# Kernel optimization log

Hardware: AMD Instinct MI355X
Metric: run time of the kernel (lower is better)

The kernel has to match this reference:

```python
import jax, jax.numpy as jnp
import numpy as np

ALG = 8  # octonion algebra dimension
_TRIPLES = [(1,2,3),(1,4,5),(1,7,6),(2,4,6),(2,5,7),(3,4,7),(3,6,5)]

def _oct_table():
    # Cayley multiplication table: e_i * e_j = S[i,j] * e_{K[i,j]}
    K = np.zeros((8,8), np.int64); S = np.zeros((8,8), np.int64)
    K[0,:] = np.arange(8); S[0,:] = 1
    K[:,0] = np.arange(8); S[:,0] = 1
    for i in range(1,8):
        K[i,i] = 0; S[i,i] = -1
    for (a,b,c) in _TRIPLES:
        for x,y,z in ((a,b,c),(b,c,a),(c,a,b)):
            K[x,y] = z; S[x,y] = 1
            K[y,x] = z; S[y,x] = -1
    return K, S

_K, _S = _oct_table()

def _ternary(w):
    # BitNet-style absmean ternary quantization (STE is irrelevant for fwd)
    scale = jnp.mean(jnp.abs(w)) + 1e-8
    wq = jnp.clip(jnp.round(w / scale), -1.0, 1.0) * scale
    return w + jax.lax.stop_gradient(wq - w)

def _oct_big(w):
    # w: [8, din8, dout8] -> structured dense [8*din8, 8*dout8]
    # out_k = sum_{i,j: e_i e_j = s e_k} s * x_i @ W_j  (64 static blocks)
    din8, dout8 = w.shape[1], w.shape[2]
    big = jnp.zeros((8, din8, 8, dout8), w.dtype)
    for i in range(8):
        for j in range(8):
            big = big.at[i, :, int(_K[i, j]), :].set(float(_S[i, j]) * w[j])
    return big.reshape(8 * din8, 8 * dout8)

def _oct_linear(x, w):
    return x @ _oct_big(_ternary(w))

def setup_inputs() -> dict:
    key = jax.random.key(0)
    k1, k2, k3, k4 = jax.random.split(key, 4)
    B, T, D = 8, 4096, 768
    H = 2048  # int(2*4*768/3) rounded up to multiple of 8
    d8, h8 = D // ALG, H // ALG
    x = jax.random.normal(k1, (B, T, D), dtype=jnp.float32)
    w_gate = 0.02 * jax.random.normal(k2, (ALG, d8, h8), dtype=jnp.float32)
    w_up   = 0.02 * jax.random.normal(k3, (ALG, d8, h8), dtype=jnp.float32)
    w_down = 0.02 * jax.random.normal(k4, (ALG, h8, d8), dtype=jnp.float32)
    return {"x": x, "w_gate": w_gate, "w_up": w_up, "w_down": w_down}

def reference(x, w_gate, w_up, w_down):
    gate = _oct_linear(x, w_gate)          # [B,T,H]
    up   = _oct_linear(x, w_up)            # [B,T,H]
    h    = jax.nn.silu(gate) * up          # SwiGLU gate
    return _oct_linear(h, w_down)          # [B,T,D]
```

## Files before the change

kernel.cpp:

```cpp
#include <hip/hip_runtime.h>
#include <hip/hip_bf16.h>

typedef unsigned short u16;
typedef unsigned int u32;
typedef float f32x4 __attribute__((ext_vector_type(4)));
typedef __bf16 bf16x8 __attribute__((ext_vector_type(8)));

#define AS1 __attribute__((address_space(1)))
#define AS3 __attribute__((address_space(3)))

#define MTOT 32768
#define DK   768
#define HN   2048

__constant__ signed char J_TAB[64] = {
  0,1,2,3,4,5,6,7,
  1,0,3,2,5,4,7,6,
  2,3,0,1,6,7,4,5,
  3,2,1,0,7,6,5,4,
  4,5,6,7,0,1,2,3,
  5,4,7,6,1,0,3,2,
  6,7,4,5,2,3,0,1,
  7,6,5,4,3,2,1,0};
__constant__ signed char S_TAB[64] = {
   1, 1, 1, 1, 1, 1, 1, 1,
  -1, 1,-1, 1,-1, 1, 1,-1,
  -1, 1, 1,-1,-1,-1, 1, 1,
  -1,-1, 1, 1,-1, 1,-1, 1,
  -1, 1, 1, 1, 1,-1,-1,-1,
  -1,-1, 1,-1, 1, 1, 1,-1,
  -1,-1,-1, 1, 1,-1, 1, 1,
  -1, 1,-1,-1, 1, 1,-1, 1};

__device__ __forceinline__ u16 f2bf(float f) {
  u32 x = __float_as_uint(f);
  x += 0x7fffu + ((x >> 16) & 1u);
  return (u16)(x >> 16);
}

__device__ __forceinline__ void gload_lds16(const void* g, void* l) {
  __builtin_amdgcn_global_load_lds((AS1 void*)(g), (AS3 void*)(l), 16, 0, 0);
}

#define PVMW(N) do { __builtin_amdgcn_sched_barrier(0); \
  asm volatile("s_waitcnt vmcnt(" #N ")" ::: "memory"); \
  __builtin_amdgcn_sched_barrier(0); } while (0)
#define PBAR() do { __builtin_amdgcn_sched_barrier(0); \
  __builtin_amdgcn_s_barrier(); \
  __builtin_amdgcn_sched_barrier(0); } while (0)
#define VMW(N) asm volatile("s_waitcnt vmcnt(" #N ")" ::: "memory")
#define BAR() __builtin_amdgcn_s_barrier()

template <int LDK>
__device__ __forceinline__ void stage_half(const u16* __restrict__ src,
                                           u16* lds, int tid) {
#pragma unroll
  for (int f0 = 0; f0 < 1024; f0 += 512) {
    int flat = f0 + tid;
    int row = flat >> 3;
    int c = (flat & 7) ^ (row & 7);
    gload_lds16(src + row * LDK + c * 8, lds + (f0 + (tid & ~63)) * 8);
  }
}

template <int LDK, bool SA, bool SB, int VM>
__device__ __forceinline__ void ktile4(
    const u16* lAp, const u16* lBp, u16* lAn, u16* lBn,
    const u16* __restrict__ aStage, const u16* __restrict__ bStage,
    int tid, int arow, int brow, int c0, int c1, f32x4 (&acc)[8][4]) {
  bf16x8 a0[4], a1[4], a2[4], a3[4], b0[4], b1[4];
#pragma unroll
  for (int mi = 0; mi < 4; ++mi)
    a0[mi] = *(const bf16x8*)(lAp + (arow + mi * 16) * 64 + c0);
#pragma unroll
  for (int ni = 0; ni < 4; ++ni)
    b0[ni] = *(const bf16x8*)(lBp + (brow + ni * 16) * 64 + c0);
#pragma unroll
  for (int mi = 0; mi < 4; ++mi)
    a1[mi] = *(const bf16x8*)(lAp + (arow + mi * 16) * 64 + c1);
#pragma unroll
  for (int ni = 0; ni < 4; ++ni)
    b1[ni] = *(const bf16x8*)(lBp + (brow + ni * 16) * 64 + c1);
  if constexpr (SA) stage_half<LDK>(aStage, lAn, tid);
  PBAR();
  __builtin_amdgcn_s_setprio(1);
#pragma unroll
  for (int mi = 0; mi < 4; ++mi)
#pragma unroll
    for (int ni = 0; ni < 4; ++ni)
      acc[mi][ni] = __builtin_amdgcn_mfma_f32_16x16x32_bf16(
          a0[mi], b0[ni], acc[mi][ni], 0, 0, 0);
  __builtin_amdgcn_s_setprio(0);
  PBAR();
#pragma unroll
  for (int mi = 0; mi < 4; ++mi)
    a2[mi] = *(const bf16x8*)(lAp + (arow + 64 + mi * 16) * 64 + c0);
  if constexpr (SA) stage_half<LDK>(aStage + 128 * LDK, lAn + 128 * 64, tid);
  PBAR();
  __builtin_amdgcn_s_setprio(1);
#pragma unroll
  for (int mi = 0; mi < 4; ++mi)
#pragma unroll
    for (int ni = 0; ni < 4; ++ni)
      acc[mi][ni] = __builtin_amdgcn_mfma_f32_16x16x32_bf16(
          a1[mi], b1[ni], acc[mi][ni], 0, 0, 0);
  __builtin_amdgcn_s_setprio(0);
  PBAR();
#pragma unroll
  for (int mi = 0; mi < 4; ++mi)
    a3[mi] = *(const bf16x8*)(lAp + (arow + 64 + mi * 16) * 64 + c1);
  if constexpr (SB) stage_half<LDK>(bStage, lBn, tid);
  PBAR();
  __builtin_amdgcn_s_setprio(1);
#pragma unroll
  for (int mi = 0; mi < 4; ++mi)
#pragma unroll
    for (int ni = 0; ni < 4; ++ni)
      acc[4 + mi][ni] = __builtin_amdgcn_mfma_f32_16x16x32_bf16(
          a2[mi], b0[ni], acc[4 + mi][ni], 0, 0, 0);
  __builtin_amdgcn_s_setprio(0);
  PBAR();
  if constexpr (SB) stage_half<LDK>(bStage + 128 * LDK, lBn + 128 * 64, tid);
  if constexpr (VM == 4) PVMW(4);
  else if constexpr (VM == 0) PVMW(0);
  PBAR();
  __builtin_amdgcn_s_setprio(1);
#pragma unroll
  for (int mi = 0; mi < 4; ++mi)
#pragma unroll
    for (int ni = 0; ni < 4; ++ni)
      acc[4 + mi][ni] = __builtin_amdgcn_mfma_f32_16x16x32_bf16(
          a3[mi], b1[ni], acc[4 + mi][ni], 0, 0, 0);
  __builtin_amdgcn_s_setprio(0);
  PBAR();
}

template <int NK, int LDK>
__device__ __forceinline__ void gemm_core(const u16* __restrict__ aSrc,
                                          const u16* __restrict__ bSrc, int tid,
                                          u16* lA0, u16* lA1, u16* lB0, u16* lB1,
                                          f32x4 (&acc)[8][4]) {
  const int lane = tid & 63;
  const int wave = tid >> 6;
  const int wm = wave >> 2, wn = wave & 3;
  const int l15 = lane & 15, quad = (lane >> 4) & 3;
  const int arow = wm * 128 + l15;
  const int brow = wn * 64 + l15;
  const int c0 = (quad ^ (l15 & 7)) * 8;
  const int c1 = ((quad + 4) ^ (l15 & 7)) * 8;

  stage_half<LDK>(aSrc, lA0, tid);
  stage_half<LDK>(aSrc + 128 * LDK, lA0 + 128 * 64, tid);
  stage_half<LDK>(bSrc, lB0, tid);
  stage_half<LDK>(bSrc + 128 * LDK, lB0 + 128 * 64, tid);
  stage_half<LDK>(bSrc + 64, lB1, tid);
  stage_half<LDK>(bSrc + 64 + 128 * LDK, lB1 + 128 * 64, tid);
  PVMW(4);
  PBAR();

#pragma unroll 1
  for (int i = 0; i < NK / 2 - 1; ++i) {
    ktile4<LDK, true, true, 4>(lA0, lB0, lA1, lB0,
                               aSrc + (2 * i + 1) * 64, bSrc + (2 * i + 2) * 64,
                               tid, arow, brow, c0, c1, acc);
    ktile4<LDK, true, true, 4>(lA1, lB1, lA0, lB1,
                               aSrc + (2 * i + 2) * 64, bSrc + (2 * i + 3) * 64,
                               tid, arow, brow, c0, c1, acc);
  }
  ktile4<LDK, true, false, 0>(lA0, lB0, lA1, lB0,
                              aSrc + (NK - 1) * 64, nullptr,
                              tid, arow, brow, c0, c1, acc);
  ktile4<LDK, false, false, -1>(lA1, lB1, lA0, lB1, nullptr, nullptr,
                                tid, arow, brow, c0, c1, acc);
}

__device__ __forceinline__ int sw3(int r) { return (r ^ (r >> 2)) & 3; }

__device__ __forceinline__ void stage_b32(const u16* __restrict__ src,
                                          u16* lds, int tid) {
#pragma unroll
  for (int f0 = 0; f0 < 1024; f0 += 256) {
    int flat = f0 + tid;
    int row = flat >> 2;
    int c = (flat & 3) ^ sw3(row);
    gload_lds16(src + (size_t)row * HN + c * 8, lds + (f0 + (tid & ~63)) * 8);
  }
}

template <bool STG, bool ANXT, int VM>
__device__ __forceinline__ void ktile_g2(
    const u16* lBread, u16* lBwrite,
    const u16* __restrict__ bStage, const u16* __restrict__ aNxtSrc,
    bf16x8 (&aCur)[4], bf16x8 (&aNxt)[4],
    int tid, int brow, int quad, f32x4 (&acc)[4][4]) {
  bf16x8 bf[4];
#pragma unroll
  for (int ni = 0; ni < 4; ++ni) {
    int row = brow + ni * 16;
    bf[ni] = *(const bf16x8*)(lBread + row * 32 + (quad ^ sw3(row)) * 8);
  }
  if constexpr (STG) stage_b32(bStage, lBwrite, tid);
  if constexpr (ANXT) {
#pragma unroll
    for (int mi = 0; mi < 4; ++mi)
      aNxt[mi] = *(const bf16x8*)(aNxtSrc + (size_t)mi * 16 * HN);
  }
  __builtin_amdgcn_s_setprio(1);
#pragma unroll
  for (int mi = 0; mi < 4; ++mi)
#pragma unroll
    for (int ni = 0; ni < 4; ++ni)
      acc[mi][ni] = __builtin_amdgcn_mfma_f32_16x16x32_bf16(
          aCur[mi], bf[ni], acc[mi][ni], 0, 0, 0);
  __builtin_amdgcn_s_setprio(0);
  if constexpr (VM == 8) VMW(8);
  else if constexpr (VM == 0) VMW(0);
  BAR();
}

__global__ void scales1_kernel(const float* __restrict__ w0,
                               const float* __restrict__ w1,
                               const float* __restrict__ w2,
                               float* __restrict__ partials) {
  __shared__ float red[256];
  const int t = blockIdx.x / 192;
  const int chunk = blockIdx.x % 192;
  const float* w = (t == 0) ? w0 : (t == 1) ? w1 : w2;
  const float4* w4 = (const float4*)(w + chunk * 1024);
  float4 v = w4[threadIdx.x];
  red[threadIdx.x] = fabsf(v.x) + fabsf(v.y) + fabsf(v.z) + fabsf(v.w);
  __syncthreads();
  for (int off = 128; off; off >>= 1) {
    if (threadIdx.x < off) red[threadIdx.x] += red[threadIdx.x + off];
    __syncthreads();
  }
  if (threadIdx.x == 0) partials[blockIdx.x] = red[0];
}

__global__ void scales2_kernel(const float* __restrict__ partials,
                               float* __restrict__ scales) {
  __shared__ float red[256];
  float s = (threadIdx.x < 192) ? partials[blockIdx.x * 192 + threadIdx.x] : 0.f;
  red[threadIdx.x] = s;
  __syncthreads();
  for (int off = 128; off; off >>= 1) {
    if (threadIdx.x < off) red[threadIdx.x] += red[threadIdx.x + off];
    __syncthreads();
  }
  if (threadIdx.x == 0) scales[blockIdx.x] = red[0] / 196608.f + 1e-8f;
}

__global__ void build_big_kernel(const float* __restrict__ w,
                                 const float* __restrict__ scales, int sidx,
                                 int A, int B, int ilv, u16* __restrict__ dst) {
  int idx = blockIdx.x * 256 + threadIdx.x;
  int K8 = 8 * A;
  int n = idx / K8;
  int k = idx - n * K8;
  int i = k / A, a = k - i * A;
  int c = n / B, b = n - c * B;
  float scale = scales[sidx];
  int j = J_TAB[i * 8 + c];
  float q = rintf(w[(j * A + a) * B + b] / scale);
  q = fminf(1.f, fmaxf(-1.f, q));
  int nd = (ilv >= 0) ? (((n & ~15) << 1) | (ilv << 4) | (n & 15)) : n;
  int kd = (ilv == -2) ? ((k & ~31) | ((k & 15) << 1) | ((k >> 4) & 1)) : k;
  dst[nd * K8 + kd] = f2bf(q * (float)S_TAB[i * 8 + c]);
}

__global__ void cvt_x_kernel(const float* __restrict__ x, u16* __restrict__ xb) {
  int gid = blockIdx.x * 256 + threadIdx.x;
  const float4* x4 = (const float4*)x;
  float4 v0 = x4[gid * 2], v1 = x4[gid * 2 + 1];
  uint4 o;
  o.x = (u32)f2bf(v0.x) | ((u32)f2bf(v0.y) << 16);
  o.y = (u32)f2bf(v0.z) | ((u32)f2bf(v0.w) << 16);
  o.z = (u32)f2bf(v1.x) | ((u32)f2bf(v1.y) << 16);
  o.w = (u32)f2bf(v1.z) | ((u32)f2bf(v1.w) << 16);
  ((uint4*)xb)[gid] = o;
}

__global__ __launch_bounds__(512, 2) void gemm1_kernel(
    const u16* __restrict__ xb, const u16* __restrict__ wgu,
    const float* __restrict__ scales, u16* __restrict__ h) {
  __shared__ __align__(16) u16 lA0[256 * 64], lA1[256 * 64];
  __shared__ __align__(16) u16 lB0[256 * 64], lB1[256 * 64];
  const int tid = threadIdx.x;
  const int logical = (blockIdx.x & 7) * 256 + (blockIdx.x >> 3);
  const int bn = logical & 15;
  const int bm = logical >> 4;
  const int m0 = bm * 256, n0 = bn * 256;

  f32x4 acc[8][4] = {};
  gemm_core<12, DK>(xb + (size_t)m0 * DK, wgu + (size_t)n0 * DK, tid,
                    lA0, lA1, lB0, lB1, acc);

  const int lane = tid & 63, wave = tid >> 6;
  const int wm = wave >> 2, wn = wave & 3;
  const int l15 = lane & 15, quad = lane >> 4;
  const float sg = scales[0], su = scales[1];
  const int a_ = bn * 4 + wn;
  u32* h32 = (u32*)h;
#pragma unroll
  for (int mi = 0; mi < 8; ++mi)
#pragma unroll
    for (int r = 0; r < 4; ++r) {
      int m = m0 + wm * 128 + mi * 16 + quad * 4 + r;
      float g0 = acc[mi][0][r] * sg, u0 = acc[mi][1][r] * su;
      float g1 = acc[mi][2][r] * sg, u1 = acc[mi][3][r] * su;
      float h0 = g0 / (1.f + __expf(-g0)) * u0;
      float h1 = g1 / (1.f + __expf(-g1)) * u1;
      h32[(size_t)m * (HN / 2) + a_ * 16 + l15] =
          (u32)f2bf(h0) | ((u32)f2bf(h1) << 16);
    }
}

__global__ __launch_bounds__(256, 2) void gemm2_kernel(
    const u16* __restrict__ h, const u16* __restrict__ wd,
    const float* __restrict__ scales, float* __restrict__ out) {
  __shared__ __align__(16) u16 lB[3][256 * 32];
  const int tid = threadIdx.x;
  const int logical = (blockIdx.x & 7) * 192 + (blockIdx.x >> 3);
  const int bn = logical % 3;
  const int bm = logical / 3;
  const int m0 = bm * 64, n0 = bn * 256;

  const int lane = tid & 63, wave = tid >> 6;
  const int l15 = lane & 15, quad = (lane >> 4) & 3;
  const int brow = wave * 64 + l15;
  const u16* bSrc = wd + (size_t)n0 * HN;
  const u16* aBase = h + (size_t)(m0 + l15) * HN + quad * 8;

  f32x4 acc[4][4] = {};
  bf16x8 aA[4], aB[4];

  stage_b32(bSrc, lB[0], tid);
  stage_b32(bSrc + 32, lB[1], tid);
#pragma unroll
  for (int mi = 0; mi < 4; ++mi)
    aA[mi] = *(const bf16x8*)(aBase + (size_t)mi * 16 * HN);
  VMW(8);
  BAR();

  u16 *q0 = lB[0], *q1 = lB[1], *q2 = lB[2];
#pragma unroll 1
  for (int it = 0; it < 31; ++it) {
    const int T = 2 * it;
    ktile_g2<true, true, 8>(q0, q2, bSrc + (T + 2) * 32,
                            aBase + (T + 1) * 32, aA, aB, tid, brow, quad, acc);
    ktile_g2<true, true, 8>(q1, q0, bSrc + (T + 3) * 32,
                            aBase + (T + 2) * 32, aB, aA, tid, brow, quad, acc);
    u16* t = q0; q0 = q2; q2 = q1; q1 = t;
  }
  ktile_g2<false, true, 8>(q0, nullptr, nullptr, aBase + 63 * 32,
                           aA, aB, tid, brow, quad, acc);
  ktile_g2<false, false, -1>(q1, nullptr, nullptr, nullptr,
                             aB, aA, tid, brow, quad, acc);

  const float sd = scales[2];
#pragma unroll
  for (int mi = 0; mi < 4; ++mi)
#pragma unroll
    for (int ni = 0; ni < 4; ++ni) {
      const int n = n0 + wave * 64 + ni * 16 + l15;
#pragma unroll
      for (int r = 0; r < 4; ++r) {
        int m = m0 + mi * 16 + quad * 4 + r;
        out[(size_t)m * DK + n] = acc[mi][ni][r] * sd;
      }
    }
}

extern "C" void kernel_launch(void* const* d_in, const int* in_sizes, int n_in,
                              void* d_out, int out_size, void* d_ws, size_t ws_size,
                              hipStream_t stream) {
  const float* x      = (const float*)d_in[0];
  const float* w_gate = (const float*)d_in[1];
  const float* w_up   = (const float*)d_in[2];
  const float* w_down = (const float*)d_in[3];
  float* out = (float*)d_out;

  char* ws = (char*)d_ws;
  float* scales   = (float*)ws;
  float* partials = (float*)(ws + 256);
  u16* wgu = (u16*)(ws + 4096);
  u16* wd  = (u16*)(ws + 4096 + 6291456u);
  u16* xb  = (u16*)(ws + 4096 + 9437184u);
  u16* h   = (u16*)(ws + 4096 + 9437184u + 50331648u);

  scales1_kernel<<<576, 256, 0, stream>>>(w_gate, w_up, w_down, partials);
  scales2_kernel<<<3, 256, 0, stream>>>(partials, scales);
  build_big_kernel<<<6144, 256, 0, stream>>>(w_gate, scales, 0, 96, 256, 0, wgu);
  build_big_kernel<<<6144, 256, 0, stream>>>(w_up,   scales, 1, 96, 256, 1, wgu);
  build_big_kernel<<<6144, 256, 0, stream>>>(w_down, scales, 2, 256, 96, -2, wd);
  cvt_x_kernel<<<12288, 256, 0, stream>>>(x, xb);
  gemm1_kernel<<<2048, 512, 0, stream>>>(xb, wgu, scales, h);
  gemm2_kernel<<<1536, 256, 0, stream>>>(h, wd, scales, out);
}
```

Baseline: 675.0 us.

## Restructure down-projection GEMM into square 128x128 tiles with LDS-staged A and B

Replaces the 64x256 down-projection tile with a 128x128 tile and a 2x2 wave layout. Both activation and weight tiles are now staged into swizzled LDS through global_load_lds, where before A was read straight from global into registers. The loop becomes a simple single-buffered stage, barrier, MFMA, barrier sequence with no prefetch overlap, and launch bounds rise to 3 blocks per CU. This is meant to improve operand reuse and occupancy, at the cost of exposing global-load latency that the old triple-buffered pipeline hid.

```diff
diff --git a/kernel.cpp b/kernel.cpp
--- a/kernel.cpp
+++ b/kernel.cpp
@@ -48,8 +48,6 @@
 #define PBAR() do { __builtin_amdgcn_sched_barrier(0); \
   __builtin_amdgcn_s_barrier(); \
   __builtin_amdgcn_sched_barrier(0); } while (0)
-#define VMW(N) asm volatile("s_waitcnt vmcnt(" #N ")" ::: "memory")
-#define BAR() __builtin_amdgcn_s_barrier()
 
 template <int LDK>
 __device__ __forceinline__ void stage_half(const u16* __restrict__ src,
@@ -60,6 +58,18 @@
     int row = flat >> 3;
     int c = (flat & 7) ^ (row & 7);
     gload_lds16(src + row * LDK + c * 8, lds + (f0 + (tid & ~63)) * 8);
+  }
+}
+
+template <int LDK>
+__device__ __forceinline__ void stage_tile256(const u16* __restrict__ src,
+                                              u16* lds, int tid) {
+#pragma unroll
+  for (int f0 = 0; f0 < 1024; f0 += 256) {
+    int flat = f0 + tid;
+    int row = flat >> 3;
+    int c = (flat & 7) ^ (row & 7);
+    gload_lds16(src + (size_t)row * LDK + c * 8, lds + (f0 + (tid & 192)) * 8);
   }
 }
 
@@ -172,50 +182,6 @@
                               tid, arow, brow, c0, c1, acc);
   ktile4<LDK, false, false, -1>(lA1, lB1, lA0, lB1, nullptr, nullptr,
                                 tid, arow, brow, c0, c1, acc);
-}
-
-__device__ __forceinline__ int sw3(int r) { return (r ^ (r >> 2)) & 3; }
-
-__device__ __forceinline__ void stage_b32(const u16* __restrict__ src,
-                                          u16* lds, int tid) {
-#pragma unroll
-  for (int f0 = 0; f0 < 1024; f0 += 256) {
-    int flat = f0 + tid;
-    int row = flat >> 2;
-    int c = (flat & 3) ^ sw3(row);
-    gload_lds16(src + (size_t)row * HN + c * 8, lds + (f0 + (tid & ~63)) * 8);
-  }
-}
-
-template <bool STG, bool ANXT, int VM>
-__device__ __forceinline__ void ktile_g2(
-    const u16* lBread, u16* lBwrite,
-    const u16* __restrict__ bStage, const u16* __restrict__ aNxtSrc,
-    bf16x8 (&aCur)[4], bf16x8 (&aNxt)[4],
-    int tid, int brow, int quad, f32x4 (&acc)[4][4]) {
-  bf16x8 bf[4];
-#pragma unroll
-  for (int ni = 0; ni < 4; ++ni) {
-    int row = brow + ni * 16;
-    bf[ni] = *(const bf16x8*)(lBread + row * 32 + (quad ^ sw3(row)) * 8);
-  }
-  if constexpr (STG) stage_b32(bStage, lBwrite, tid);
-  if constexpr (ANXT) {
-#pragma unroll
-    for (int mi = 0; mi < 4; ++mi)
-      aNxt[mi] = *(const bf16x8*)(aNxtSrc + (size_t)mi * 16 * HN);
-  }
-  __builtin_amdgcn_s_setprio(1);
-#pragma unroll
-  for (int mi = 0; mi < 4; ++mi)
-#pragma unroll
-    for (int ni = 0; ni < 4; ++ni)
-      acc[mi][ni] = __builtin_amdgcn_mfma_f32_16x16x32_bf16(
-          aCur[mi], bf[ni], acc[mi][ni], 0, 0, 0);
-  __builtin_amdgcn_s_setprio(0);
-  if constexpr (VM == 8) VMW(8);
-  else if constexpr (VM == 0) VMW(0);
-  BAR();
 }
 
 __global__ void scales1_kernel(const float* __restrict__ w0,
@@ -315,57 +281,63 @@
     }
 }
 
-__global__ __launch_bounds__(256, 2) void gemm2_kernel(
+__global__ __launch_bounds__(256, 3) void gemm2_kernel(
     const u16* __restrict__ h, const u16* __restrict__ wd,
     const float* __restrict__ scales, float* __restrict__ out) {
-  __shared__ __align__(16) u16 lB[3][256 * 32];
+  __shared__ __align__(16) u16 lA[128 * 64];
+  __shared__ __align__(16) u16 lB[128 * 64];
   const int tid = threadIdx.x;
   const int logical = (blockIdx.x & 7) * 192 + (blockIdx.x >> 3);
-  const int bn = logical % 3;
-  const int bm = logical / 3;
-  const int m0 = bm * 64, n0 = bn * 256;
+  const int bn = logical % 6;
+  const int bm = logical / 6;
+  const int m0 = bm * 128, n0 = bn * 128;
+  const u16* aSrc = h + (size_t)m0 * HN;
+  const u16* bSrc = wd + (size_t)n0 * HN;
 
   const int lane = tid & 63, wave = tid >> 6;
+  const int wm = wave >> 1, wn = wave & 1;
   const int l15 = lane & 15, quad = (lane >> 4) & 3;
-  const int brow = wave * 64 + l15;
-  const u16* bSrc = wd + (size_t)n0 * HN;
-  const u16* aBase = h + (size_t)(m0 + l15) * HN + quad * 8;
+  const int arow = wm * 64 + l15;
+  const int brow = wn * 64 + l15;
+  const int c0 = (quad ^ (l15 & 7)) * 8;
+  const int c1 = ((quad + 4) ^ (l15 & 7)) * 8;
 
   f32x4 acc[4][4] = {};
-  bf16x8 aA[4], aB[4];
-
-  stage_b32(bSrc, lB[0], tid);
-  stage_b32(bSrc + 32, lB[1], tid);
-#pragma unroll
-  for (int mi = 0; mi < 4; ++mi)
-    aA[mi] = *(const bf16x8*)(aBase + (size_t)mi * 16 * HN);
-  VMW(8);
-  BAR();
-
-  u16 *q0 = lB[0], *q1 = lB[1], *q2 = lB[2];
+
 #pragma unroll 1
-  for (int it = 0; it < 31; ++it) {
-    const int T = 2 * it;
-    ktile_g2<true, true, 8>(q0, q2, bSrc + (T + 2) * 32,
-                            aBase + (T + 1) * 32, aA, aB, tid, brow, quad, acc);
-    ktile_g2<true, true, 8>(q1, q0, bSrc + (T + 3) * 32,
-                            aBase + (T + 2) * 32, aB, aA, tid, brow, quad, acc);
-    u16* t = q0; q0 = q2; q2 = q1; q1 = t;
-  }
-  ktile_g2<false, true, 8>(q0, nullptr, nullptr, aBase + 63 * 32,
-                           aA, aB, tid, brow, quad, acc);
-  ktile_g2<false, false, -1>(q1, nullptr, nullptr, nullptr,
-                             aB, aA, tid, brow, quad, acc);
+  for (int S = 0; S < HN / 64; ++S) {
+    stage_tile256<HN>(aSrc + S * 64, lA, tid);
+    stage_tile256<HN>(bSrc + S * 64, lB, tid);
+    __syncthreads();
+#pragma unroll
+    for (int k = 0; k < 2; ++k) {
+      const int ck = k ? c1 : c0;
+      bf16x8 af[4], bf[4];
+#pragma unroll
+      for (int mi = 0; mi < 4; ++mi)
+        af[mi] = *(const bf16x8*)(lA + (arow + mi * 16) * 64 + ck);
+#pragma unroll
+      for (int ni = 0; ni < 4; ++ni)
+        bf[ni] = *(const bf16x8*)(lB + (brow + ni * 16) * 64 + ck);
+#pragma unroll
+      for (int mi = 0; mi < 4; ++mi)
+#pragma unroll
+        for (int ni = 0; ni < 4; ++ni)
+          acc[mi][ni] = __builtin_amdgcn_mfma_f32_16x16x32_bf16(
+              af[mi], bf[ni], acc[mi][ni], 0, 0, 0);
+    }
+    __syncthreads();
+  }
 
   const float sd = scales[2];
 #pragma unroll
   for (int mi = 0; mi < 4; ++mi)
 #pragma unroll
     for (int ni = 0; ni < 4; ++ni) {
-      const int n = n0 + wave * 64 + ni * 16 + l15;
+      const int n = n0 + wn * 64 + ni * 16 + l15;
 #pragma unroll
       for (int r = 0; r < 4; ++r) {
-        int m = m0 + mi * 16 + quad * 4 + r;
+        int m = m0 + wm * 64 + mi * 16 + quad * 4 + r;
         out[(size_t)m * DK + n] = acc[mi][ni][r] * sd;
       }
     }
```

Result: faster. 565.4 us (-16.2%).
